# Optimization experiments

Hardware: AMD Instinct MI355X
Metric: run time of the kernel (lower is better)

The kernel has to match this reference:

```python
import jax, jax.numpy as jnp
import numpy as np

TOP_K = 2
NORM_TOPK_PROB = True


def setup_inputs() -> dict:
    key = jax.random.key(0)
    k1, k2, k3 = jax.random.split(key, 3)
    B, S, H, E = 4, 2048, 2048, 8
    hidden_states = jax.random.normal(k1, (B, S, H), dtype=jnp.float32)
    gate_w = jax.random.normal(k2, (E, H), dtype=jnp.float32) * 0.02   # nn.Linear weight [E, H]
    expert_w = jax.random.normal(k3, (E, H, H), dtype=jnp.float32) * 0.02  # per-expert Linear weight [H_out, H_in]
    return {"hidden_states": hidden_states, "gate_w": gate_w, "expert_w": expert_w}


def reference(hidden_states, gate_w, expert_w):
    B, S, H = hidden_states.shape
    E = gate_w.shape[0]
    x = hidden_states.reshape(-1, H)                      # [T, H], T = B*S
    T = x.shape[0]

    router_logits = x @ gate_w.T                          # [T, E]
    probs = jax.nn.softmax(router_logits.astype(jnp.float32), axis=-1)
    top_w, top_i = jax.lax.top_k(probs, TOP_K)            # [T, K]
    if NORM_TOPK_PROB:
        top_w = top_w / jnp.sum(top_w, axis=-1, keepdims=True)
    top_w = top_w.astype(x.dtype)

    # dense [T, E] combine weights (scatter of top-k weights)
    w_full = jnp.zeros((T, E), dtype=x.dtype).at[jnp.arange(T)[:, None], top_i].add(top_w)

    # expert_i(x) = x @ W_i.T  (bias-free Linear)
    expert_out = jnp.einsum('th,eoh->eto', x, expert_w)   # [E, T, H]
    out = jnp.einsum('te,eto->to', w_full, expert_out)    # [T, H]

    return out.reshape(B, S, H), router_logits.reshape(B, S, E)
```

## Files before the change

kernel.cpp:

```cpp
#include <hip/hip_runtime.h>
#include <stdint.h>

#define T_TOK 8192
#define HDIM  2048
#define NEXP  8
#define BM    256
#define BN    256
#define BK    64
#define RTOK  32

typedef __bf16 bf16x8 __attribute__((ext_vector_type(8)));
typedef float  f32x4  __attribute__((ext_vector_type(4)));
typedef unsigned short u16;
typedef u16    u16x8  __attribute__((ext_vector_type(8)));

typedef const __attribute__((address_space(1))) void* gptr_t;
typedef __attribute__((address_space(3))) void* lptr_t;

static __device__ __forceinline__ u16 f2bf(float f) {
    union { float f; unsigned u; } v; v.f = f;
    unsigned u = v.u;
    u = (u + 0x7FFFu + ((u >> 16) & 1u)) >> 16;
    return (u16)u;
}

__global__ __launch_bounds__(256) void cvt_kernel(const float* __restrict__ in,
                                                  u16* __restrict__ out, int n8) {
    int i = blockIdx.x * 256 + threadIdx.x;
    if (i >= n8) return;
    const float4* p = (const float4*)in + (size_t)i * 2;
    float4 a = p[0], b = p[1];
    u16x8 r;
    r[0] = f2bf(a.x); r[1] = f2bf(a.y); r[2] = f2bf(a.z); r[3] = f2bf(a.w);
    r[4] = f2bf(b.x); r[5] = f2bf(b.y); r[6] = f2bf(b.z); r[7] = f2bf(b.w);
    ((u16x8*)out)[i] = r;
}

__global__ __launch_bounds__(256) void router_kernel(const float* __restrict__ x,
                                                     const float* __restrict__ gw,
                                                     u16* __restrict__ xb,
                                                     float* __restrict__ logits_out,
                                                     int* __restrict__ cnt,
                                                     int* __restrict__ rows,
                                                     float* __restrict__ wts) {
    __shared__ int   lcnt[NEXP];
    __shared__ int   lbase[NEXP];
    __shared__ int   lrows[NEXP][RTOK];
    __shared__ float lwtsS[NEXP][RTOK];

    int tid  = threadIdx.x;
    int lane = tid & 63;
    int wave = tid >> 6;
    if (tid < NEXP) lcnt[tid] = 0;
    __syncthreads();

    int t0 = blockIdx.x * RTOK + wave * 8;
    const float4* g4 = (const float4*)gw;

    float acc[8][NEXP] = {};
    #pragma unroll
    for (int i = 0; i < HDIM / 4 / 64; i++) {
        int idx = lane + i * 64;
        float4 gv[NEXP];
        #pragma unroll
        for (int e = 0; e < NEXP; e++) gv[e] = g4[e * (HDIM / 4) + idx];
        #pragma unroll
        for (int tk = 0; tk < 8; tk++) {
            int t = t0 + tk;
            float4 xv = ((const float4*)(x + (size_t)t * HDIM))[idx];
            ushort4 h;
            h.x = f2bf(xv.x); h.y = f2bf(xv.y); h.z = f2bf(xv.z); h.w = f2bf(xv.w);
            ((ushort4*)(xb + (size_t)t * HDIM))[idx] = h;
            #pragma unroll
            for (int e = 0; e < NEXP; e++)
                acc[tk][e] += xv.x * gv[e].x + xv.y * gv[e].y +
                              xv.z * gv[e].z + xv.w * gv[e].w;
        }
    }
    #pragma unroll
    for (int tk = 0; tk < 8; tk++)
        #pragma unroll
        for (int e = 0; e < NEXP; e++)
            #pragma unroll
            for (int off = 32; off > 0; off >>= 1)
                acc[tk][e] += __shfl_xor(acc[tk][e], off, 64);

    if (lane == 0) {
        #pragma unroll
        for (int tk = 0; tk < 8; tk++) {
            int t = t0 + tk;
            #pragma unroll
            for (int e = 0; e < NEXP; e++) logits_out[(size_t)t * NEXP + e] = acc[tk][e];
            int e0 = 0;
            #pragma unroll
            for (int e = 1; e < NEXP; e++) if (acc[tk][e] > acc[tk][e0]) e0 = e;
            int e1 = (e0 == 0) ? 1 : 0;
            #pragma unroll
            for (int e = 0; e < NEXP; e++)
                if (e != e0 && acc[tk][e] > acc[tk][e1]) e1 = e;
            float w0 = 1.0f / (1.0f + expf(acc[tk][e1] - acc[tk][e0]));
            int p0 = atomicAdd(&lcnt[e0], 1);
            lrows[e0][p0] = t; lwtsS[e0][p0] = w0;
            int p1 = atomicAdd(&lcnt[e1], 1);
            lrows[e1][p1] = t; lwtsS[e1][p1] = 1.0f - w0;
        }
    }
    __syncthreads();
    if (tid < NEXP) lbase[tid] = atomicAdd(&cnt[tid], lcnt[tid]);
    __syncthreads();
    int e = tid >> 5, j = tid & 31;
    if (j < lcnt[e]) {
        int b = lbase[e] + j;
        rows[e * T_TOK + b] = lrows[e][j];
        wts[e * T_TOK + b]  = lwtsS[e][j];
    }
}

__global__ __launch_bounds__(512, 2) void moe_gemm(const u16* __restrict__ xb,
                                                   const u16* __restrict__ wb,
                                                   const int* __restrict__ cnt,
                                                   const int* __restrict__ rows,
                                                   const float* __restrict__ wts,
                                                   float* __restrict__ out) {
    int p  = blockIdx.x;
    int xc = p & 7;
    int q  = p >> 3;
    int rt = q & 31;
    int g  = (q >> 5) * 8 + xc;
    int e  = g >> 3;
    int nb = (g & 7) * BN;

    int count = cnt[e];
    int rowBase = rt * BM;
    if (rowBase >= count) return;

    const u16*   W     = wb  + (size_t)e * HDIM * HDIM;
    const int*   rlist = rows + e * T_TOK;
    const float* wlist = wts  + e * T_TOK;

    __shared__ u16 As[2][BM * BK];
    __shared__ u16 Bs[2][BM * BK];

    int tid  = threadIdx.x;
    int lane = tid & 63;
    int wave = tid >> 6;
    int wr = wave >> 2, wc = wave & 3;

    const u16* a_src[4];
    const u16* b_src[4];
    #pragma unroll
    for (int l = 0; l < 4; l++) {
        int row  = (tid >> 3) + l * 64;
        int clog = (tid & 7) ^ (row & 7);
        int tok  = rlist[min(rowBase + row, count - 1)];
        a_src[l] = xb + (size_t)tok * HDIM + clog * 8;
        b_src[l] = W + (size_t)(nb + row) * HDIM + clog * 8;
    }
    int wslot = (tid & ~63);

    auto stage = [&](u16* A_lds, u16* B_lds, int kb) {
        #pragma unroll
        for (int l = 0; l < 4; l++) {
            __builtin_amdgcn_global_load_lds((gptr_t)(a_src[l] + kb),
                                             (lptr_t)(A_lds + (l * 512 + wslot) * 8),
                                             16, 0, 0);
            __builtin_amdgcn_global_load_lds((gptr_t)(b_src[l] + kb),
                                             (lptr_t)(B_lds + (l * 512 + wslot) * 8),
                                             16, 0, 0);
        }
    };

    int lrow = lane & 15;
    int kq   = lane >> 4;
    int mloc[8], nloc[4];
    #pragma unroll
    for (int i = 0; i < 8; i++) mloc[i] = wr * 128 + i * 16 + lrow;
    #pragma unroll
    for (int j = 0; j < 4; j++) nloc[j] = wc * 64 + j * 16 + lrow;

    f32x4 acc[8][4] = {};

    auto compute = [&](const u16* A_lds, const u16* B_lds) {
        #pragma unroll
        for (int s = 0; s < 2; s++) {
            int chunk = s * 4 + kq;
            bf16x8 a[8], b[4];
            #pragma unroll
            for (int i = 0; i < 8; i++) {
                int aslot = (mloc[i] << 3) | (chunk ^ (mloc[i] & 7));
                a[i] = *(const bf16x8*)(A_lds + aslot * 8);
            }
            #pragma unroll
            for (int j = 0; j < 4; j++) {
                int bslot = (nloc[j] << 3) | (chunk ^ (nloc[j] & 7));
                b[j] = *(const bf16x8*)(B_lds + bslot * 8);
            }
            #pragma unroll
            for (int i = 0; i < 8; i++)
                #pragma unroll
                for (int j = 0; j < 4; j++)
                    acc[i][j] = __builtin_amdgcn_mfma_f32_16x16x32_bf16(
                                    a[i], b[j], acc[i][j], 0, 0, 0);
        }
    };

    stage(As[0], Bs[0], 0);
    stage(As[1], Bs[1], BK);

    for (int kb = 0; kb < HDIM - 2 * BK; kb += 2 * BK) {
        asm volatile("s_waitcnt vmcnt(8)" ::: "memory");
        __builtin_amdgcn_sched_barrier(0);
        __builtin_amdgcn_s_barrier();
        compute(As[0], Bs[0]);
        __builtin_amdgcn_sched_barrier(0);
        __builtin_amdgcn_s_barrier();
        stage(As[0], Bs[0], kb + 2 * BK);

        asm volatile("s_waitcnt vmcnt(8)" ::: "memory");
        __builtin_amdgcn_sched_barrier(0);
        __builtin_amdgcn_s_barrier();
        compute(As[1], Bs[1]);
        __builtin_amdgcn_sched_barrier(0);
        __builtin_amdgcn_s_barrier();
        stage(As[1], Bs[1], kb + 3 * BK);
    }
    asm volatile("s_waitcnt vmcnt(8)" ::: "memory");
    __builtin_amdgcn_sched_barrier(0);
    __builtin_amdgcn_s_barrier();
    compute(As[0], Bs[0]);
    asm volatile("s_waitcnt vmcnt(0)" ::: "memory");
    __builtin_amdgcn_sched_barrier(0);
    __builtin_amdgcn_s_barrier();
    compute(As[1], Bs[1]);

    int srow = (lane >> 4) * 4;
    #pragma unroll
    for (int i = 0; i < 8; i++) {
        #pragma unroll
        for (int r = 0; r < 4; r++) {
            int row = rowBase + wr * 128 + i * 16 + srow + r;
            if (row < count) {
                int   tok = rlist[row];
                float wgt = wlist[row];
                #pragma unroll
                for (int j = 0; j < 4; j++) {
                    int col = nb + wc * 64 + j * 16 + lrow;
                    atomicAdd(out + (size_t)tok * HDIM + col, wgt * acc[i][j][r]);
                }
            }
        }
    }
}

extern "C" void kernel_launch(void* const* d_in, const int* in_sizes, int n_in,
                              void* d_out, int out_size, void* d_ws, size_t ws_size,
                              hipStream_t stream) {
    const float* x  = (const float*)d_in[0];
    const float* gw = (const float*)d_in[1];
    const float* ew = (const float*)d_in[2];
    float* out    = (float*)d_out;
    float* logits = out + (size_t)T_TOK * HDIM;

    char* ws = (char*)d_ws;
    int*   cnt  = (int*)ws;
    int*   rows = (int*)(ws + 1024);
    float* wts  = (float*)(ws + 1024 + 262144);
    u16*   xb   = (u16*)(ws + 1024 + 2 * 262144);
    u16*   wb   = xb + (size_t)T_TOK * HDIM;

    hipMemsetAsync(d_out, 0, (size_t)T_TOK * HDIM * sizeof(float), stream);
    hipMemsetAsync(cnt, 0, NEXP * sizeof(int), stream);

    int nw8 = NEXP * HDIM * HDIM / 8;
    cvt_kernel<<<(nw8 + 255) / 256, 256, 0, stream>>>(ew, wb, nw8);

    router_kernel<<<T_TOK / RTOK, 256, 0, stream>>>(x, gw, xb, logits, cnt, rows, wts);

    moe_gemm<<<NEXP * 32 * 8, 512, 0, stream>>>(xb, wb, cnt, rows, wts, out);
}
```

Baseline: 618.9 us.

## Restructure MoE GEMM main loop into split A/B staging with B held in registers

Splits the LDS tiles into two 128-row halves and stages the A and B tiles at different points of each K period, so global-to-LDS loads for the next tile are issued mid-compute rather than after a full compute block. B fragments are loaded into registers once per period, and A fragments are read in small two-row phases interleaved with MFMAs, with s_setprio raising wave priority during the MFMA bursts. The aim is to overlap memory traffic and LDS reads with matrix math and to cut LDS read pressure. It adds more barriers per period and more register use for the held B fragments, which may lower occupancy.

```diff
diff --git a/kernel.cpp b/kernel.cpp
--- a/kernel.cpp
+++ b/kernel.cpp
@@ -138,100 +138,109 @@
     const int*   rlist = rows + e * T_TOK;
     const float* wlist = wts  + e * T_TOK;
 
-    __shared__ u16 As[2][BM * BK];
-    __shared__ u16 Bs[2][BM * BK];
+    __shared__ u16 As[2][2][128 * BK];
+    __shared__ u16 Bs[2][2][128 * BK];
 
     int tid  = threadIdx.x;
     int lane = tid & 63;
     int wave = tid >> 6;
     int wr = wave >> 2, wc = wave & 3;
-
-    const u16* a_src[4];
-    const u16* b_src[4];
-    #pragma unroll
-    for (int l = 0; l < 4; l++) {
-        int row  = (tid >> 3) + l * 64;
-        int clog = (tid & 7) ^ (row & 7);
-        int tok  = rlist[min(rowBase + row, count - 1)];
-        a_src[l] = xb + (size_t)tok * HDIM + clog * 8;
-        b_src[l] = W + (size_t)(nb + row) * HDIM + clog * 8;
-    }
-    int wslot = (tid & ~63);
-
-    auto stage = [&](u16* A_lds, u16* B_lds, int kb) {
-        #pragma unroll
-        for (int l = 0; l < 4; l++) {
-            __builtin_amdgcn_global_load_lds((gptr_t)(a_src[l] + kb),
-                                             (lptr_t)(A_lds + (l * 512 + wslot) * 8),
-                                             16, 0, 0);
-            __builtin_amdgcn_global_load_lds((gptr_t)(b_src[l] + kb),
-                                             (lptr_t)(B_lds + (l * 512 + wslot) * 8),
-                                             16, 0, 0);
-        }
+    int wslot = tid & ~63;
+
+    const u16* a_src[2][2];
+    const u16* b_src[2][2];
+    int clog = ((tid & 7) ^ ((tid >> 3) & 7)) * 8;
+    #pragma unroll
+    for (int h = 0; h < 2; h++)
+        #pragma unroll
+        for (int l = 0; l < 2; l++) {
+            int row = h * 128 + l * 64 + (tid >> 3);
+            int tok = rlist[min(rowBase + row, count - 1)];
+            a_src[h][l] = xb + (size_t)tok * HDIM + clog;
+            b_src[h][l] = W + (size_t)(nb + row) * HDIM + clog;
+        }
+
+    auto stageA = [&](int d, int h, int kb) {
+        #pragma unroll
+        for (int l = 0; l < 2; l++)
+            __builtin_amdgcn_global_load_lds((gptr_t)(a_src[h][l] + kb),
+                (lptr_t)(&As[d][h][(l * 512 + wslot) * 8]), 16, 0, 0);
+    };
+    auto stageB = [&](int d, int h, int kb) {
+        #pragma unroll
+        for (int l = 0; l < 2; l++)
+            __builtin_amdgcn_global_load_lds((gptr_t)(b_src[h][l] + kb),
+                (lptr_t)(&Bs[d][h][(l * 512 + wslot) * 8]), 16, 0, 0);
     };
 
     int lrow = lane & 15;
     int kq   = lane >> 4;
-    int mloc[8], nloc[4];
-    #pragma unroll
-    for (int i = 0; i < 8; i++) mloc[i] = wr * 128 + i * 16 + lrow;
-    #pragma unroll
-    for (int j = 0; j < 4; j++) nloc[j] = wc * 64 + j * 16 + lrow;
-
-    f32x4 acc[8][4] = {};
-
-    auto compute = [&](const u16* A_lds, const u16* B_lds) {
-        #pragma unroll
-        for (int s = 0; s < 2; s++) {
-            int chunk = s * 4 + kq;
-            bf16x8 a[8], b[4];
-            #pragma unroll
-            for (int i = 0; i < 8; i++) {
-                int aslot = (mloc[i] << 3) | (chunk ^ (mloc[i] & 7));
-                a[i] = *(const bf16x8*)(A_lds + aslot * 8);
+
+    f32x4  acc[8][4] = {};
+    bf16x8 breg[4][2];
+
+    auto loadB = [&](int C) {
+        #pragma unroll
+        for (int j = 0; j < 4; j++)
+            #pragma unroll
+            for (int s = 0; s < 2; s++) {
+                int col = (wc & 1) * 64 + j * 16 + lrow;
+                breg[j][s] = *(const bf16x8*)(&Bs[C][wc >> 1]
+                    [(size_t)(((col) << 3) | ((s * 4 + kq) ^ (col & 7))) * 8]);
             }
-            #pragma unroll
-            for (int j = 0; j < 4; j++) {
-                int bslot = (nloc[j] << 3) | (chunk ^ (nloc[j] & 7));
-                b[j] = *(const bf16x8*)(B_lds + bslot * 8);
-            }
-            #pragma unroll
-            for (int i = 0; i < 8; i++)
-                #pragma unroll
-                for (int j = 0; j < 4; j++)
-                    acc[i][j] = __builtin_amdgcn_mfma_f32_16x16x32_bf16(
-                                    a[i], b[j], acc[i][j], 0, 0, 0);
-        }
     };
 
-    stage(As[0], Bs[0], 0);
-    stage(As[1], Bs[1], BK);
+#define MPHASE(C, I0) do {                                                     \
+    bf16x8 a0_[2], a1_[2];                                                     \
+    _Pragma("unroll") for (int s = 0; s < 2; s++) {                            \
+        int r0 = (I0) * 16 + lrow, r1 = ((I0) + 1) * 16 + lrow;                \
+        a0_[s] = *(const bf16x8*)(&As[C][wr]                                   \
+            [(size_t)((r0 << 3) | ((s * 4 + kq) ^ (r0 & 7))) * 8]);            \
+        a1_[s] = *(const bf16x8*)(&As[C][wr]                                   \
+            [(size_t)((r1 << 3) | ((s * 4 + kq) ^ (r1 & 7))) * 8]);            \
+    }                                                                          \
+    __builtin_amdgcn_s_setprio(1);                                             \
+    _Pragma("unroll") for (int j = 0; j < 4; j++)                              \
+        _Pragma("unroll") for (int s = 0; s < 2; s++) {                        \
+            acc[(I0)][j]     = __builtin_amdgcn_mfma_f32_16x16x32_bf16(        \
+                                   a0_[s], breg[j][s], acc[(I0)][j], 0, 0, 0); \
+            acc[(I0) + 1][j] = __builtin_amdgcn_mfma_f32_16x16x32_bf16(        \
+                                   a1_[s], breg[j][s], acc[(I0) + 1][j], 0, 0, 0); \
+        }                                                                      \
+    __builtin_amdgcn_s_setprio(0);                                             \
+} while (0)
+
+#define PERIOD(C, KB, SA, SB, VN) do {                                         \
+    asm volatile("s_waitcnt vmcnt(" #VN ") lgkmcnt(0)" ::: "memory");          \
+    __builtin_amdgcn_sched_barrier(0);                                         \
+    __builtin_amdgcn_s_barrier();                                              \
+    __builtin_amdgcn_sched_barrier(0);                                         \
+    if (SA) { stageA(1 - (C), 0, (KB) + BK); stageA(1 - (C), 1, (KB) + BK); }  \
+    loadB(C);                                                                  \
+    MPHASE(C, 0);                                                              \
+    asm volatile("s_waitcnt lgkmcnt(0)" ::: "memory");                         \
+    __builtin_amdgcn_sched_barrier(0);                                         \
+    __builtin_amdgcn_s_barrier();                                              \
+    __builtin_amdgcn_sched_barrier(0);                                         \
+    if (SB) { stageB(C, 0, (KB) + 2 * BK); stageB(C, 1, (KB) + 2 * BK); }      \
+    MPHASE(C, 2);                                                              \
+    MPHASE(C, 4);                                                              \
+    MPHASE(C, 6);                                                              \
+} while (0)
+
+    stageA(0, 0, 0);  stageA(0, 1, 0);
+    stageB(0, 0, 0);  stageB(0, 1, 0);
+    stageB(1, 0, BK); stageB(1, 1, BK);
 
     for (int kb = 0; kb < HDIM - 2 * BK; kb += 2 * BK) {
-        asm volatile("s_waitcnt vmcnt(8)" ::: "memory");
-        __builtin_amdgcn_sched_barrier(0);
-        __builtin_amdgcn_s_barrier();
-        compute(As[0], Bs[0]);
-        __builtin_amdgcn_sched_barrier(0);
-        __builtin_amdgcn_s_barrier();
-        stage(As[0], Bs[0], kb + 2 * BK);
-
-        asm volatile("s_waitcnt vmcnt(8)" ::: "memory");
-        __builtin_amdgcn_sched_barrier(0);
-        __builtin_amdgcn_s_barrier();
-        compute(As[1], Bs[1]);
-        __builtin_amdgcn_sched_barrier(0);
-        __builtin_amdgcn_s_barrier();
-        stage(As[1], Bs[1], kb + 3 * BK);
-    }
-    asm volatile("s_waitcnt vmcnt(8)" ::: "memory");
-    __builtin_amdgcn_sched_barrier(0);
-    __builtin_amdgcn_s_barrier();
-    compute(As[0], Bs[0]);
-    asm volatile("s_waitcnt vmcnt(0)" ::: "memory");
-    __builtin_amdgcn_sched_barrier(0);
-    __builtin_amdgcn_s_barrier();
-    compute(As[1], Bs[1]);
+        PERIOD(0, kb, 1, 1, 4);
+        PERIOD(1, kb + BK, 1, 1, 4);
+    }
+    PERIOD(0, HDIM - 2 * BK, 1, 0, 4);
+    PERIOD(1, HDIM - BK, 0, 0, 0);
+
+#undef PERIOD
+#undef MPHASE
 
     int srow = (lane >> 4) * 4;
     #pragma unroll
```

Result: no change. 607.3 us (-1.9%).

## Shrink MoE GEMM tiles to 128x256x32 and raise occupancy to four blocks per CU

Applied to the files above, without the earlier changes.

Halves the row tile and the K step of the grouped expert GEMM. This cuts the accumulator count per thread from 32 to 16 fragments and the LDS footprint, so launch bounds can request four blocks per CU. The staging, the LDS swizzle and the block-to-expert mapping are rewritten to match. The aim is less wasted work on partially filled row tiles and better latency hiding through occupancy. In exchange, each loaded tile is reused less, and there are twice as many barriers per K and more blocks.

```diff
diff --git a/kernel.cpp b/kernel.cpp
--- a/kernel.cpp
+++ b/kernel.cpp
@@ -4,9 +4,9 @@
 #define T_TOK 8192
 #define HDIM  2048
 #define NEXP  8
-#define BM    256
+#define BM    128
 #define BN    256
-#define BK    64
+#define BK    32
 #define RTOK  32
 
 typedef __bf16 bf16x8 __attribute__((ext_vector_type(8)));
@@ -116,7 +116,7 @@
     }
 }
 
-__global__ __launch_bounds__(512, 2) void moe_gemm(const u16* __restrict__ xb,
+__global__ __launch_bounds__(512, 4) void moe_gemm(const u16* __restrict__ xb,
                                                    const u16* __restrict__ wb,
                                                    const int* __restrict__ cnt,
                                                    const int* __restrict__ rows,
@@ -125,10 +125,9 @@
     int p  = blockIdx.x;
     int xc = p & 7;
     int q  = p >> 3;
-    int rt = q & 31;
-    int g  = (q >> 5) * 8 + xc;
-    int e  = g >> 3;
-    int nb = (g & 7) * BN;
+    int rt = q & 63;
+    int e  = q >> 6;
+    int nb = xc * BN;
 
     int count = cnt[e];
     int rowBase = rt * BM;
@@ -139,92 +138,80 @@
     const float* wlist = wts  + e * T_TOK;
 
     __shared__ u16 As[2][BM * BK];
-    __shared__ u16 Bs[2][BM * BK];
+    __shared__ u16 Bs[2][BN * BK];
 
     int tid  = threadIdx.x;
     int lane = tid & 63;
     int wave = tid >> 6;
     int wr = wave >> 2, wc = wave & 3;
-
-    const u16* a_src[4];
-    const u16* b_src[4];
-    #pragma unroll
-    for (int l = 0; l < 4; l++) {
-        int row  = (tid >> 3) + l * 64;
-        int clog = (tid & 7) ^ (row & 7);
-        int tok  = rlist[min(rowBase + row, count - 1)];
-        a_src[l] = xb + (size_t)tok * HDIM + clog * 8;
-        b_src[l] = W + (size_t)(nb + row) * HDIM + clog * 8;
-    }
-    int wslot = (tid & ~63);
-
-    auto stage = [&](u16* A_lds, u16* B_lds, int kb) {
-        #pragma unroll
-        for (int l = 0; l < 4; l++) {
-            __builtin_amdgcn_global_load_lds((gptr_t)(a_src[l] + kb),
-                                             (lptr_t)(A_lds + (l * 512 + wslot) * 8),
-                                             16, 0, 0);
+    int wslot = tid & ~63;
+
+    int clog = ((tid & 3) ^ ((tid >> 3) & 3)) * 8;
+    int arow = tid >> 2;
+    int atok = rlist[min(rowBase + arow, count - 1)];
+    const u16* a_src = xb + (size_t)atok * HDIM + clog;
+    const u16* b_src[2];
+    #pragma unroll
+    for (int l = 0; l < 2; l++)
+        b_src[l] = W + (size_t)(nb + l * 128 + (tid >> 2)) * HDIM + clog;
+
+    auto stage = [&](int d, int kb) {
+        __builtin_amdgcn_global_load_lds((gptr_t)(a_src + kb),
+            (lptr_t)(&As[d][(size_t)tid * 8]), 16, 0, 0);
+        #pragma unroll
+        for (int l = 0; l < 2; l++)
             __builtin_amdgcn_global_load_lds((gptr_t)(b_src[l] + kb),
-                                             (lptr_t)(B_lds + (l * 512 + wslot) * 8),
-                                             16, 0, 0);
-        }
+                (lptr_t)(&Bs[d][(size_t)(l * 512 + wslot + lane) * 8]), 16, 0, 0);
     };
 
     int lrow = lane & 15;
     int kq   = lane >> 4;
-    int mloc[8], nloc[4];
-    #pragma unroll
-    for (int i = 0; i < 8; i++) mloc[i] = wr * 128 + i * 16 + lrow;
-    #pragma unroll
-    for (int j = 0; j < 4; j++) nloc[j] = wc * 64 + j * 16 + lrow;
-
-    f32x4 acc[8][4] = {};
+
+    f32x4 acc[4][4] = {};
 
     auto compute = [&](const u16* A_lds, const u16* B_lds) {
-        #pragma unroll
-        for (int s = 0; s < 2; s++) {
-            int chunk = s * 4 + kq;
-            bf16x8 a[8], b[4];
-            #pragma unroll
-            for (int i = 0; i < 8; i++) {
-                int aslot = (mloc[i] << 3) | (chunk ^ (mloc[i] & 7));
-                a[i] = *(const bf16x8*)(A_lds + aslot * 8);
-            }
-            #pragma unroll
-            for (int j = 0; j < 4; j++) {
-                int bslot = (nloc[j] << 3) | (chunk ^ (nloc[j] & 7));
-                b[j] = *(const bf16x8*)(B_lds + bslot * 8);
-            }
-            #pragma unroll
-            for (int i = 0; i < 8; i++)
-                #pragma unroll
-                for (int j = 0; j < 4; j++)
-                    acc[i][j] = __builtin_amdgcn_mfma_f32_16x16x32_bf16(
-                                    a[i], b[j], acc[i][j], 0, 0, 0);
-        }
+        bf16x8 a[4], b[4];
+        #pragma unroll
+        for (int i = 0; i < 4; i++) {
+            int r = wr * 64 + i * 16 + lrow;
+            int aslot = (r << 2) | (kq ^ ((r >> 1) & 3));
+            a[i] = *(const bf16x8*)(A_lds + (size_t)aslot * 8);
+        }
+        #pragma unroll
+        for (int j = 0; j < 4; j++) {
+            int c = wc * 64 + j * 16 + lrow;
+            int bslot = (c << 2) | (kq ^ ((c >> 1) & 3));
+            b[j] = *(const bf16x8*)(B_lds + (size_t)bslot * 8);
+        }
+        #pragma unroll
+        for (int i = 0; i < 4; i++)
+            #pragma unroll
+            for (int j = 0; j < 4; j++)
+                acc[i][j] = __builtin_amdgcn_mfma_f32_16x16x32_bf16(
+                                a[i], b[j], acc[i][j], 0, 0, 0);
     };
 
-    stage(As[0], Bs[0], 0);
-    stage(As[1], Bs[1], BK);
+    stage(0, 0);
+    stage(1, BK);
 
     for (int kb = 0; kb < HDIM - 2 * BK; kb += 2 * BK) {
-        asm volatile("s_waitcnt vmcnt(8)" ::: "memory");
+        asm volatile("s_waitcnt vmcnt(3)" ::: "memory");
         __builtin_amdgcn_sched_barrier(0);
         __builtin_amdgcn_s_barrier();
         compute(As[0], Bs[0]);
         __builtin_amdgcn_sched_barrier(0);
         __builtin_amdgcn_s_barrier();
-        stage(As[0], Bs[0], kb + 2 * BK);
-
-        asm volatile("s_waitcnt vmcnt(8)" ::: "memory");
+        stage(0, kb + 2 * BK);
+
+        asm volatile("s_waitcnt vmcnt(3)" ::: "memory");
         __builtin_amdgcn_sched_barrier(0);
         __builtin_amdgcn_s_barrier();
         compute(As[1], Bs[1]);
         __builtin_amdgcn_sched_barrier(0);
         __builtin_amdgcn_s_barrier();
-        stage(As[1], Bs[1], kb + 3 * BK);
-    }
-    asm volatile("s_waitcnt vmcnt(8)" ::: "memory");
+        stage(1, kb + 3 * BK);
+    }
+    asm volatile("s_waitcnt vmcnt(3)" ::: "memory");
     __builtin_amdgcn_sched_barrier(0);
     __builtin_amdgcn_s_barrier();
     compute(As[0], Bs[0]);
@@ -235,10 +222,10 @@
 
     int srow = (lane >> 4) * 4;
     #pragma unroll
-    for (int i = 0; i < 8; i++) {
+    for (int i = 0; i < 4; i++) {
         #pragma unroll
         for (int r = 0; r < 4; r++) {
-            int row = rowBase + wr * 128 + i * 16 + srow + r;
+            int row = rowBase + wr * 64 + i * 16 + srow + r;
             if (row < count) {
                 int   tok = rlist[row];
                 float wgt = wlist[row];
@@ -276,5 +263,5 @@
 
     router_kernel<<<T_TOK / RTOK, 256, 0, stream>>>(x, gw, xb, logits, cnt, rows, wts);
 
-    moe_gemm<<<NEXP * 32 * 8, 512, 0, stream>>>(xb, wb, cnt, rows, wts, out);
-}
+    moe_gemm<<<NEXP * 64 * 8, 512, 0, stream>>>(xb, wb, cnt, rows, wts, out);
+}
```

Result: no change. 617.7 us (-0.2%).
